# Kernel optimization log

Measured on AMD Instinct MI355X. Metric: run time of the kernel, lower is better.

## Reference

```python
import jax, jax.numpy as jnp
import numpy as np

DIM = 1024
NUM_HEADS = 16
HEAD_DIM = DIM // NUM_HEADS
SCALE = HEAD_DIM ** -0.5


def setup_inputs() -> dict:
    key = jax.random.key(0)
    k1, k2, k3 = jax.random.split(key, 3)
    B, N = 4, 2048
    x = jax.random.normal(k1, (B, N, DIM), dtype=jnp.float32)
    W_qkv = jax.random.normal(k2, (DIM, 3 * DIM), dtype=jnp.float32) * (DIM ** -0.5)
    b_qkv = jnp.zeros((3 * DIM,), dtype=jnp.float32)
    W_proj = jax.random.normal(k3, (DIM, DIM), dtype=jnp.float32) * (DIM ** -0.5)
    b_proj = jnp.zeros((DIM,), dtype=jnp.float32)
    return {"x": x, "W_qkv": W_qkv, "b_qkv": b_qkv, "W_proj": W_proj, "b_proj": b_proj}


def reference(x, W_qkv, b_qkv, W_proj, b_proj):
    B, N, D = x.shape
    qkv = x @ W_qkv + b_qkv                       # [B, N, 3D]
    qkv = qkv.reshape(B, N, 3, NUM_HEADS, HEAD_DIM)
    qkv = jnp.transpose(qkv, (2, 0, 3, 1, 4))     # [3, B, H, N, hd]
    q, k, v = qkv[0], qkv[1], qkv[2]
    attn = jnp.einsum('bhnd,bhmd->bhnm', q, k) * SCALE
    attn = jax.nn.softmax(attn, axis=-1)
    out = jnp.einsum('bhnm,bhmd->bhnd', attn, v)  # [B, H, N, hd]
    out = jnp.transpose(out, (0, 2, 1, 3)).reshape(B, N, D)
    return out @ W_proj + b_proj
```

## Files before the change

kernel.cpp:

```cpp
#include <hip/hip_runtime.h>
#include <hip/hip_bf16.h>

#define BATCH 4
#define SEQ   2048
#define DIM   1024
#define NHEAD 16
#define HDIM  64
#define ROWS  (BATCH * SEQ)
#define LS    68
#define GLS   68
#define QSCALE 0.18033688011f

typedef __bf16 bf16x8 __attribute__((ext_vector_type(8)));
typedef float  f32x4  __attribute__((ext_vector_type(4)));
typedef float  f32x16 __attribute__((ext_vector_type(16)));

static __device__ __forceinline__ uint pack2(float a, float b) {
    ushort ua = __builtin_bit_cast(ushort, (__bf16)a);
    ushort ub = __builtin_bit_cast(ushort, (__bf16)b);
    return (uint)ua | ((uint)ub << 16);
}
#define PLSWAP(a, b) asm volatile("v_permlane32_swap_b32 %0, %1" : "+v"(a), "+v"(b))

__global__ __launch_bounds__(256)
void convert_bf16_kernel(const float* __restrict__ in, ushort* __restrict__ out, int n8) {
    int stride = gridDim.x * blockDim.x;
    for (int i = blockIdx.x * blockDim.x + threadIdx.x; i < n8; i += stride) {
        float4 a = ((const float4*)in)[2 * i];
        float4 b = ((const float4*)in)[2 * i + 1];
        ushort u[8];
        u[0] = __builtin_bit_cast(ushort, (__bf16)a.x);
        u[1] = __builtin_bit_cast(ushort, (__bf16)a.y);
        u[2] = __builtin_bit_cast(ushort, (__bf16)a.z);
        u[3] = __builtin_bit_cast(ushort, (__bf16)a.w);
        u[4] = __builtin_bit_cast(ushort, (__bf16)b.x);
        u[5] = __builtin_bit_cast(ushort, (__bf16)b.y);
        u[6] = __builtin_bit_cast(ushort, (__bf16)b.z);
        u[7] = __builtin_bit_cast(ushort, (__bf16)b.w);
        ((uint4*)out)[i] = *(uint4*)u;
    }
}

__global__ __launch_bounds__(256)
void transpose_bf16_kernel(const float* __restrict__ W, ushort* __restrict__ Wt,
                           int K, int N) {
    __shared__ float tile[32][33];
    const int tx = threadIdx.x, ty = threadIdx.y;
    const int n0 = blockIdx.x * 32, k0 = blockIdx.y * 32;
#pragma unroll
    for (int i = 0; i < 4; ++i)
        tile[ty + 8 * i][tx] = W[(long)(k0 + ty + 8 * i) * N + n0 + tx];
    __syncthreads();
#pragma unroll
    for (int i = 0; i < 4; ++i) {
        float v = tile[tx][ty + 8 * i];
        Wt[(long)(n0 + ty + 8 * i) * K + k0 + tx] = __builtin_bit_cast(ushort, (__bf16)v);
    }
}

__global__ __launch_bounds__(256)
void gemm_mfma_kernel(const ushort* __restrict__ A, const ushort* __restrict__ Bt,
                      const float* __restrict__ bias,
                      int M, int N, int K, int mode,
                      __hip_bfloat16* __restrict__ Qb,
                      __hip_bfloat16* __restrict__ Kb,
                      __hip_bfloat16* __restrict__ Vb,
                      float* __restrict__ Cout) {
    const int t  = threadIdx.x;
    const int w  = t >> 6;
    const int l  = t & 63;
    const int c  = l & 15;
    const int g  = l >> 4;
    const int wr = w >> 1, wc = w & 1;
    const int row0 = blockIdx.y * 128;
    const int col0 = blockIdx.x * 128;

    __shared__ ushort As[128][GLS];
    __shared__ ushort Bs[128][GLS];

    const int sr = t >> 3;
    const int sa = t & 7;

    f32x4 acc[4][4];
#pragma unroll
    for (int i = 0; i < 4; ++i)
#pragma unroll
        for (int j = 0; j < 4; ++j) acc[i][j] = (f32x4){0.f, 0.f, 0.f, 0.f};

    for (int k0 = 0; k0 < K; k0 += 64) {
        __syncthreads();
#pragma unroll
        for (int i = 0; i < 4; ++i) {
            int row = i * 32 + sr;
            uint4 a = *(const uint4*)(A + (size_t)(row0 + row) * K + k0 + 8 * sa);
            *(uint2*)&As[row][8 * sa]     = make_uint2(a.x, a.y);
            *(uint2*)&As[row][8 * sa + 4] = make_uint2(a.z, a.w);
            uint4 b = *(const uint4*)(Bt + (size_t)(col0 + row) * K + k0 + 8 * sa);
            *(uint2*)&Bs[row][8 * sa]     = make_uint2(b.x, b.y);
            *(uint2*)&Bs[row][8 * sa + 4] = make_uint2(b.z, b.w);
        }
        __syncthreads();

#pragma unroll
        for (int ks = 0; ks < 2; ++ks) {
            bf16x8 am[4], bn[4];
#pragma unroll
            for (int mt = 0; mt < 4; ++mt) {
                uint2 a0 = *(const uint2*)&As[wr * 64 + mt * 16 + c][ks * 32 + 8 * g];
                uint2 a1 = *(const uint2*)&As[wr * 64 + mt * 16 + c][ks * 32 + 8 * g + 4];
                am[mt] = __builtin_bit_cast(bf16x8, make_uint4(a0.x, a0.y, a1.x, a1.y));
            }
#pragma unroll
            for (int nt = 0; nt < 4; ++nt) {
                uint2 b0 = *(const uint2*)&Bs[wc * 64 + nt * 16 + c][ks * 32 + 8 * g];
                uint2 b1 = *(const uint2*)&Bs[wc * 64 + nt * 16 + c][ks * 32 + 8 * g + 4];
                bn[nt] = __builtin_bit_cast(bf16x8, make_uint4(b0.x, b0.y, b1.x, b1.y));
            }
#pragma unroll
            for (int mt = 0; mt < 4; ++mt)
#pragma unroll
                for (int nt = 0; nt < 4; ++nt)
                    acc[mt][nt] = __builtin_amdgcn_mfma_f32_16x16x32_bf16(
                        am[mt], bn[nt], acc[mt][nt], 0, 0, 0);
        }
    }

    float bv[4];
#pragma unroll
    for (int nt = 0; nt < 4; ++nt) bv[nt] = bias[col0 + wc * 64 + nt * 16 + c];

#pragma unroll
    for (int mt = 0; mt < 4; ++mt) {
#pragma unroll
        for (int r = 0; r < 4; ++r) {
            int grow = row0 + wr * 64 + mt * 16 + 4 * g + r;
#pragma unroll
            for (int nt = 0; nt < 4; ++nt) {
                int gcol = col0 + wc * 64 + nt * 16 + c;
                float v = acc[mt][nt][r] + bv[nt];
                if (mode == 0) {
                    int s = gcol >> 10;
                    int hc = gcol & 1023;
                    int h = hc >> 6, d = hc & 63;
                    int bi = grow >> 11, n = grow & 2047;
                    size_t off = ((size_t)(bi * NHEAD + h) * SEQ + n) * HDIM + d;
                    if (s == 0) v *= QSCALE;
                    __hip_bfloat16 hb = __float2bfloat16(v);
                    if (s == 0)      Qb[off] = hb;
                    else if (s == 1) Kb[off] = hb;
                    else             Vb[off] = hb;
                } else {
                    Cout[(size_t)grow * N + gcol] = v;
                }
            }
        }
    }
}

__global__ __launch_bounds__(256)
void attn_mfma2_kernel(const ushort* __restrict__ Qg,
                       const ushort* __restrict__ Kg,
                       const ushort* __restrict__ Vg,
                       ushort* __restrict__ O) {
    const int id  = blockIdx.x;
    const int bh  = (id & 7) * 8 + ((id >> 3) & 7);
    const int qt  = id >> 6;
    const int t   = threadIdx.x;
    const int w   = t >> 6, l = t & 63;
    const int lo5 = l & 31, hi = l >> 5;
    const size_t base = (size_t)bh * SEQ * HDIM;
    const int q0  = qt * 128 + w * 32;

    __shared__ ushort Ks[2][64 * LS];
    __shared__ ushort Vt[2][64 * LS];

    bf16x8 qf[4];
    {
        const ushort* qrow = Qg + base + (size_t)(q0 + lo5) * HDIM + 8 * hi;
#pragma unroll
        for (int db = 0; db < 4; ++db)
            qf[db] = __builtin_bit_cast(bf16x8, *(const uint4*)(qrow + 16 * db));
    }

    const int ksr = t & 63, kch = t >> 6;
    const int vkp = t & 31, vcg = t >> 5;
    const ushort* Kptr = Kg + base + (size_t)ksr * HDIM + 16 * kch;
    const ushort* Vptr = Vg + base + (size_t)(2 * vkp) * HDIM + 8 * vcg;

    uint4 kr0, kr1, vr0, vr1;
    kr0 = *(const uint4*)(Kptr);
    kr1 = *(const uint4*)(Kptr + 8);
    vr0 = *(const uint4*)(Vptr);
    vr1 = *(const uint4*)(Vptr + HDIM);

    auto stageK = [&](int buf, uint4 a, uint4 b) {
        ushort* p = &Ks[buf][ksr * LS + 16 * kch];
        *(uint2*)(p)      = make_uint2(a.x, a.y);
        *(uint2*)(p + 4)  = make_uint2(a.z, a.w);
        *(uint2*)(p + 8)  = make_uint2(b.x, b.y);
        *(uint2*)(p + 12) = make_uint2(b.z, b.w);
    };
    auto stageV = [&](int buf, uint4 a, uint4 b) {
        const uint* pa = (const uint*)&a;
        const uint* pb = (const uint*)&b;
#pragma unroll
        for (int e = 0; e < 8; ++e) {
            uint vlo = (e & 1) ? (pa[e >> 1] >> 16) : (pa[e >> 1] & 0xffffu);
            uint vhi = (e & 1) ? (pb[e >> 1] >> 16) : (pb[e >> 1] & 0xffffu);
            *(uint*)&Vt[buf][(8 * vcg + e) * LS + 2 * vkp] = vlo | (vhi << 16);
        }
    };
    stageK(0, kr0, kr1);
    stageV(0, vr0, vr1);
    __syncthreads();

    f32x16 o0, o1;
#pragma unroll
    for (int r = 0; r < 16; ++r) { o0[r] = 0.f; o1[r] = 0.f; }
    float m0 = -1e30f, ll = 0.f;

    for (int kt = 0; kt < 32; ++kt) {
        const int cur = kt & 1;
        if (kt < 31) {
            const size_t off = (size_t)(kt + 1) * 64 * HDIM;
            kr0 = *(const uint4*)(Kptr + off);
            kr1 = *(const uint4*)(Kptr + off + 8);
            vr0 = *(const uint4*)(Vptr + off);
            vr1 = *(const uint4*)(Vptr + off + HDIM);
        }

        f32x16 s[2];
        __builtin_amdgcn_s_setprio(1);
#pragma unroll
        for (int kb = 0; kb < 2; ++kb) {
            f32x16 acc;
#pragma unroll
            for (int r = 0; r < 16; ++r) acc[r] = 0.f;
#pragma unroll
            for (int db = 0; db < 4; ++db) {
                const ushort* ap = &Ks[cur][(kb * 32 + lo5) * LS + 16 * db + 8 * hi];
                uint2 a0 = *(const uint2*)(ap);
                uint2 a1 = *(const uint2*)(ap + 4);
                bf16x8 af = __builtin_bit_cast(bf16x8, make_uint4(a0.x, a0.y, a1.x, a1.y));
                acc = __builtin_amdgcn_mfma_f32_32x32x16_bf16(af, qf[db], acc, 0, 0, 0);
            }
            s[kb] = acc;
        }
        __builtin_amdgcn_s_setprio(0);

        float pmax = s[0][0];
#pragma unroll
        for (int r = 1; r < 16; ++r) pmax = fmaxf(pmax, s[0][r]);
#pragma unroll
        for (int r = 0; r < 16; ++r) pmax = fmaxf(pmax, s[1][r]);
        pmax = fmaxf(pmax, __shfl_xor(pmax, 32, 64));

        if (!__all(pmax <= m0 + 8.f)) {
            float mn = fmaxf(m0, pmax);
            float corr = __builtin_amdgcn_exp2f(m0 - mn);
#pragma unroll
            for (int r = 0; r < 16; ++r) { o0[r] *= corr; o1[r] *= corr; }
            ll *= corr;
            m0 = mn;
        }
        float rs = 0.f;
#pragma unroll
        for (int r = 0; r < 16; ++r) {
            float p = __builtin_amdgcn_exp2f(s[0][r] - m0); s[0][r] = p; rs += p;
        }
#pragma unroll
        for (int r = 0; r < 16; ++r) {
            float p = __builtin_amdgcn_exp2f(s[1][r] - m0); s[1][r] = p; rs += p;
        }
        rs += __shfl_xor(rs, 32, 64);
        ll += rs;

        bf16x8 pbf[4];
#pragma unroll
        for (int kb = 0; kb < 2; ++kb)
#pragma unroll
            for (int kk = 0; kk < 2; ++kk) {
                const int b0 = kk * 8;
                uint w0 = pack2(s[kb][b0 + 0], s[kb][b0 + 1]);
                uint w1 = pack2(s[kb][b0 + 2], s[kb][b0 + 3]);
                uint w2 = pack2(s[kb][b0 + 4], s[kb][b0 + 5]);
                uint w3 = pack2(s[kb][b0 + 6], s[kb][b0 + 7]);
                PLSWAP(w0, w2);
                PLSWAP(w1, w3);
                pbf[kb * 2 + kk] = __builtin_bit_cast(bf16x8, make_uint4(w0, w1, w2, w3));
            }

        __builtin_amdgcn_s_setprio(1);
#pragma unroll
        for (int kb = 0; kb < 2; ++kb)
#pragma unroll
            for (int kk = 0; kk < 2; ++kk) {
                const int kcol = kb * 32 + kk * 16 + 8 * hi;
                const ushort* vp0 = &Vt[cur][lo5 * LS + kcol];
                uint2 v0 = *(const uint2*)(vp0);
                uint2 v1 = *(const uint2*)(vp0 + 4);
                bf16x8 vf0 = __builtin_bit_cast(bf16x8, make_uint4(v0.x, v0.y, v1.x, v1.y));
                o0 = __builtin_amdgcn_mfma_f32_32x32x16_bf16(vf0, pbf[kb * 2 + kk], o0, 0, 0, 0);
                const ushort* vp1 = vp0 + 32 * LS;
                uint2 v2 = *(const uint2*)(vp1);
                uint2 v3 = *(const uint2*)(vp1 + 4);
                bf16x8 vf1 = __builtin_bit_cast(bf16x8, make_uint4(v2.x, v2.y, v3.x, v3.y));
                o1 = __builtin_amdgcn_mfma_f32_32x32x16_bf16(vf1, pbf[kb * 2 + kk], o1, 0, 0, 0);
            }
        __builtin_amdgcn_s_setprio(0);

        __syncthreads();
        if (kt < 31) {
            stageK(cur ^ 1, kr0, kr1);
            stageV(cur ^ 1, vr0, vr1);
        }
        __syncthreads();
    }

    const float inv = 1.f / ll;
    const int b = bh >> 4, h = bh & 15;
    ushort* orow = O + (size_t)(b * SEQ + q0 + lo5) * DIM + h * HDIM;
#pragma unroll
    for (int j = 0; j < 4; ++j) {
        uint2 st;
        st.x = pack2(o0[4 * j + 0] * inv, o0[4 * j + 1] * inv);
        st.y = pack2(o0[4 * j + 2] * inv, o0[4 * j + 3] * inv);
        *(uint2*)(orow + 8 * j + 4 * hi) = st;
        st.x = pack2(o1[4 * j + 0] * inv, o1[4 * j + 1] * inv);
        st.y = pack2(o1[4 * j + 2] * inv, o1[4 * j + 3] * inv);
        *(uint2*)(orow + 32 + 8 * j + 4 * hi) = st;
    }
}

extern "C" void kernel_launch(void* const* d_in, const int* in_sizes, int n_in,
                              void* d_out, int out_size, void* d_ws, size_t ws_size,
                              hipStream_t stream) {
    const float* x      = (const float*)d_in[0];
    const float* W_qkv  = (const float*)d_in[1];
    const float* b_qkv  = (const float*)d_in[2];
    const float* W_proj = (const float*)d_in[3];
    const float* b_proj = (const float*)d_in[4];
    float* out = (float*)d_out;

    const size_t qkv_elems = (size_t)BATCH * NHEAD * SEQ * HDIM;
    char* ws = (char*)d_ws;
    ushort* xb      = (ushort*)ws;
    ushort* Wqkv_t  = (ushort*)(ws + qkv_elems * 2);
    ushort* Wproj_t = (ushort*)(ws + qkv_elems * 2 + (size_t)DIM * 3 * DIM * 2);
    char*   ws2     = ws + qkv_elems * 2 + (size_t)DIM * 3 * DIM * 2 + (size_t)DIM * DIM * 2;
    __hip_bfloat16* Qb = (__hip_bfloat16*)ws2;
    __hip_bfloat16* Kb = (__hip_bfloat16*)(ws2 + qkv_elems * 2);
    __hip_bfloat16* Vb = (__hip_bfloat16*)(ws2 + qkv_elems * 4);
    ushort* attnout = xb;

    convert_bf16_kernel<<<2048, 256, 0, stream>>>(x, xb, ROWS * DIM / 8);
    transpose_bf16_kernel<<<dim3(3 * DIM / 32, DIM / 32), dim3(32, 8), 0, stream>>>(
        W_qkv, Wqkv_t, DIM, 3 * DIM);
    transpose_bf16_kernel<<<dim3(DIM / 32, DIM / 32), dim3(32, 8), 0, stream>>>(
        W_proj, Wproj_t, DIM, DIM);

    gemm_mfma_kernel<<<dim3(3 * DIM / 128, ROWS / 128), 256, 0, stream>>>(
        xb, Wqkv_t, b_qkv, ROWS, 3 * DIM, DIM, 0, Qb, Kb, Vb, nullptr);

    attn_mfma2_kernel<<<dim3(1024), 256, 0, stream>>>(
        (const ushort*)Qb, (const ushort*)Kb, (const ushort*)Vb, attnout);

    gemm_mfma_kernel<<<dim3(DIM / 128, ROWS / 128), 256, 0, stream>>>(
        attnout, Wproj_t, b_proj, ROWS, DIM, DIM, 1, nullptr, nullptr, nullptr, out);
}
```

Baseline: 237.7 us.

## Deepen K/V prefetch to two tiles and drop a per-iteration barrier

The attention loop now stores the already-loaded next K/V tile into the alternate LDS buffer at the start of each iteration, then issues global loads two tiles ahead. This removes one of the two __syncthreads per iteration, and the global load latency now overlaps a full iteration of compute. The V transpose staging uses a byte-permute instruction instead of shift/mask, and the max and exp-sum reductions are split across several accumulators to shorten dependency chains. Register pressure rises slightly, and correctness depends on the single remaining barrier protecting buffer reuse.

```diff
diff --git a/kernel.cpp b/kernel.cpp
--- a/kernel.cpp
+++ b/kernel.cpp
@@ -187,12 +187,6 @@
     const ushort* Kptr = Kg + base + (size_t)ksr * HDIM + 16 * kch;
     const ushort* Vptr = Vg + base + (size_t)(2 * vkp) * HDIM + 8 * vcg;
 
-    uint4 kr0, kr1, vr0, vr1;
-    kr0 = *(const uint4*)(Kptr);
-    kr1 = *(const uint4*)(Kptr + 8);
-    vr0 = *(const uint4*)(Vptr);
-    vr1 = *(const uint4*)(Vptr + HDIM);
-
     auto stageK = [&](int buf, uint4 a, uint4 b) {
         ushort* p = &Ks[buf][ksr * LS + 16 * kch];
         *(uint2*)(p)      = make_uint2(a.x, a.y);
@@ -205,13 +199,26 @@
         const uint* pb = (const uint*)&b;
 #pragma unroll
         for (int e = 0; e < 8; ++e) {
-            uint vlo = (e & 1) ? (pa[e >> 1] >> 16) : (pa[e >> 1] & 0xffffu);
-            uint vhi = (e & 1) ? (pb[e >> 1] >> 16) : (pb[e >> 1] & 0xffffu);
-            *(uint*)&Vt[buf][(8 * vcg + e) * LS + 2 * vkp] = vlo | (vhi << 16);
+            uint sel = (e & 1) ? 0x07060302u : 0x05040100u;
+            uint packed = __builtin_amdgcn_perm(pb[e >> 1], pa[e >> 1], sel);
+            *(uint*)&Vt[buf][(8 * vcg + e) * LS + 2 * vkp] = packed;
         }
     };
+
+    uint4 kr0, kr1, vr0, vr1;
+    kr0 = *(const uint4*)(Kptr);
+    kr1 = *(const uint4*)(Kptr + 8);
+    vr0 = *(const uint4*)(Vptr);
+    vr1 = *(const uint4*)(Vptr + HDIM);
     stageK(0, kr0, kr1);
     stageV(0, vr0, vr1);
+    {
+        const size_t off = (size_t)64 * HDIM;
+        kr0 = *(const uint4*)(Kptr + off);
+        kr1 = *(const uint4*)(Kptr + off + 8);
+        vr0 = *(const uint4*)(Vptr + off);
+        vr1 = *(const uint4*)(Vptr + off + HDIM);
+    }
     __syncthreads();
 
     f32x16 o0, o1;
@@ -222,7 +229,11 @@
     for (int kt = 0; kt < 32; ++kt) {
         const int cur = kt & 1;
         if (kt < 31) {
-            const size_t off = (size_t)(kt + 1) * 64 * HDIM;
+            stageK(cur ^ 1, kr0, kr1);
+            stageV(cur ^ 1, vr0, vr1);
+        }
+        if (kt < 30) {
+            const size_t off = (size_t)(kt + 2) * 64 * HDIM;
             kr0 = *(const uint4*)(Kptr + off);
             kr1 = *(const uint4*)(Kptr + off + 8);
             vr0 = *(const uint4*)(Vptr + off);
@@ -248,11 +259,14 @@
         }
         __builtin_amdgcn_s_setprio(0);
 
-        float pmax = s[0][0];
-#pragma unroll
-        for (int r = 1; r < 16; ++r) pmax = fmaxf(pmax, s[0][r]);
-#pragma unroll
-        for (int r = 0; r < 16; ++r) pmax = fmaxf(pmax, s[1][r]);
+        float c0 = s[0][0], c1 = s[0][1];
+#pragma unroll
+        for (int r = 2; r < 16; r += 2) {
+            c0 = fmaxf(fmaxf(c0, s[0][r]), s[0][r + 1]);
+            c1 = fmaxf(fmaxf(c1, s[1][r]), s[1][r + 1]);
+        }
+        c0 = fmaxf(fmaxf(c0, s[1][0]), s[1][1]);
+        float pmax = fmaxf(c0, c1);
         pmax = fmaxf(pmax, __shfl_xor(pmax, 32, 64));
 
         if (!__all(pmax <= m0 + 8.f)) {
@@ -263,15 +277,15 @@
             ll *= corr;
             m0 = mn;
         }
-        float rs = 0.f;
-#pragma unroll
-        for (int r = 0; r < 16; ++r) {
-            float p = __builtin_amdgcn_exp2f(s[0][r] - m0); s[0][r] = p; rs += p;
-        }
-#pragma unroll
-        for (int r = 0; r < 16; ++r) {
-            float p = __builtin_amdgcn_exp2f(s[1][r] - m0); s[1][r] = p; rs += p;
-        }
+        float a0 = 0.f, a1 = 0.f, a2 = 0.f, a3 = 0.f;
+#pragma unroll
+        for (int r = 0; r < 16; r += 2) {
+            float p0 = __builtin_amdgcn_exp2f(s[0][r]     - m0); s[0][r]     = p0; a0 += p0;
+            float p1 = __builtin_amdgcn_exp2f(s[0][r + 1] - m0); s[0][r + 1] = p1; a1 += p1;
+            float p2 = __builtin_amdgcn_exp2f(s[1][r]     - m0); s[1][r]     = p2; a2 += p2;
+            float p3 = __builtin_amdgcn_exp2f(s[1][r + 1] - m0); s[1][r + 1] = p3; a3 += p3;
+        }
+        float rs = (a0 + a1) + (a2 + a3);
         rs += __shfl_xor(rs, 32, 64);
         ll += rs;
 
@@ -310,11 +324,6 @@
         __builtin_amdgcn_s_setprio(0);
 
         __syncthreads();
-        if (kt < 31) {
-            stageK(cur ^ 1, kr0, kr1);
-            stageV(cur ^ 1, vr0, vr1);
-        }
-        __syncthreads();
     }
 
     const float inv = 1.f / ll;
```

New measurement: 239.0 us. About the same (+0.5%).
